# Kernel optimization log

Hardware: AMD Instinct MI355X
Metric: run time of the kernel (lower is better)

Reference implementation:

```python
import jax, jax.numpy as jnp
import numpy as np
from jax import lax

DN = ('NCDHW', 'OIDHW', 'NCDHW')
BN_EPS = 1e-5  # eval-mode BatchNorm3d with running_mean=0, running_var=1


def conv3d(x, w, b):
    y = lax.conv_general_dilated(x, w, window_strides=(1, 1, 1),
                                 padding=[(1, 1)] * 3, dimension_numbers=DN)
    return y + b[None, :, None, None, None]


def maxpool2(x):
    return lax.reduce_window(x, -jnp.inf, lax.max,
                             (1, 1, 2, 2, 2), (1, 1, 2, 2, 2), 'VALID')


def spline_block(x, cw, cb, knots, sw, w1, w2, g, beta):
    # SplineConv3d: conv -> (BSpline3D blend with SiLU) -> BN(eval) -> maxpool
    y = conv3d(x, cw, cb)                                   # [b,c,d,h,w]
    basis = jnp.maximum(y[..., None] - knots, 0.0) ** 3     # [b,c,d,h,w,k]
    sp = jnp.einsum('bcdhwk,ck->bcdhw', basis, sw)
    out = (w1[None, :, None, None, None] * sp
           + w2[None, :, None, None, None] * (y * jax.nn.sigmoid(y)))
    scale = (g / jnp.sqrt(1.0 + BN_EPS))[None, :, None, None, None]
    return maxpool2(out * scale + beta[None, :, None, None, None])


def setup_inputs() -> dict:
    key = jax.random.key(0)
    ks = iter(jax.random.split(key, 40))
    def nrm(shape, s=1.0):
        return jax.random.normal(next(ks), shape, dtype=jnp.float32) * s
    d = {}
    d['x'] = nrm((2, 1, 64, 64, 64))
    for cin, cout, t in [(1, 32, '1'), (32, 64, '2'), (64, 128, '3')]:
        d[f'c{t}_w'] = nrm((cout, cin, 3, 3, 3), 0.1)
        d[f'c{t}_b'] = nrm((cout,), 0.01)
        d[f'c{t}_knots'] = jnp.linspace(-1.0, 1.0, 10).astype(jnp.float32)
        d[f'c{t}_sw'] = nrm((cout, 10), 0.2)
        d[f'c{t}_w1'] = nrm((cout,), 0.2)
        d[f'c{t}_w2'] = nrm((cout,), 0.2)
        d[f'bn{t}_g'] = 1.0 + nrm((cout,), 0.1)
        d[f'bn{t}_b'] = nrm((cout,), 0.1)
    d['fc1_w'] = nrm((256, 128), 0.05)
    d['fc1_b'] = nrm((256,), 0.01)
    d['fc2_w'] = nrm((2, 256), 0.05)
    d['fc2_b'] = nrm((2,), 0.01)
    return d


def reference(x,
              c1_w, c1_b, c1_knots, c1_sw, c1_w1, c1_w2, bn1_g, bn1_b,
              c2_w, c2_b, c2_knots, c2_sw, c2_w1, c2_w2, bn2_g, bn2_b,
              c3_w, c3_b, c3_knots, c3_sw, c3_w1, c3_w2, bn3_g, bn3_b,
              fc1_w, fc1_b, fc2_w, fc2_b):
    h = spline_block(x, c1_w, c1_b, c1_knots, c1_sw, c1_w1, c1_w2, bn1_g, bn1_b)
    h = spline_block(h, c2_w, c2_b, c2_knots, c2_sw, c2_w1, c2_w2, bn2_g, bn2_b)
    h = spline_block(h, c3_w, c3_b, c3_knots, c3_sw, c3_w1, c3_w2, bn3_g, bn3_b)
    h = h.mean(axis=(2, 3, 4))          # AdaptiveAvgPool3d((1,1,1)) + flatten
    h = jax.nn.relu(h @ fc1_w.T + fc1_b)  # dropout is identity in eval mode
    return h @ fc2_w.T + fc2_b
```

## Files before the change

kernel.cpp:

```cpp
#include <hip/hip_runtime.h>
#include <math.h>


#define GLOBAL_AS __attribute__((address_space(1)))
#define LDS_AS    __attribute__((address_space(3)))

static __device__ __forceinline__ void async_ld16(const float* g, float* l) {
    __builtin_amdgcn_global_load_lds((const GLOBAL_AS void*)g, (LDS_AS void*)l,
                                     16, 0, 0);
}

__global__ __launch_bounds__(256) void repack_kernel(
    const float* __restrict__ w1, const float* __restrict__ w2,
    const float* __restrict__ w3,
    float* __restrict__ o1, float* __restrict__ o2, float* __restrict__ o3)
{
    const int i = blockIdx.x * 256 + threadIdx.x;
    const float* src;
    float* dst;
    if (i < 32)            { src = w1 + i * 27;           dst = o1 + i * 28; }
    else if (i < 2080)     { const int j = i - 32;   src = w2 + j * 27; dst = o2 + j * 28; }
    else if (i < 10272)    { const int j = i - 2080; src = w3 + j * 27; dst = o3 + j * 28; }
    else return;
#pragma unroll
    for (int t = 0; t < 27; t++) dst[t] = src[t];
    dst[27] = 0.0f;
}

template <int TPB_, int CIN, int CSPLIT, int G,
          int WDT, int WHT, int WWT, int BD, int BH, int BW>
__global__ __launch_bounds__(TPB_, 2) void spline_block_kernel(
    const float* __restrict__ x,
    const float4* __restrict__ wpk,
    const float* __restrict__ cb,
    const float* __restrict__ knots,
    const float* __restrict__ sw,
    const float* __restrict__ w1,
    const float* __restrict__ w2,
    const float* __restrict__ g,
    const float* __restrict__ beta,
    const float* __restrict__ zbuf,
    float* __restrict__ out,
    int N, int Cout, int D, int H, int W,
    int ntiles, int nthw, int ntw)
{
    constexpr int NSW    = BD * BH * BW;
    constexpr int NW     = TPB_ / 64;
    constexpr int CPG    = CIN / CSPLIT;
    constexpr int ID     = 2 * WDT + 2;
    constexpr int IH     = 2 * WHT + 2;
    constexpr int CHK    = (WWT + 4) / 2;
    constexpr int PITCH  = CHK * 4;
    constexpr int ROWS   = ID * IH;
    constexpr int CHUNKS = ROWS * CHK;
    constexpr int PHYS   = CHUNKS * 4;
    constexpr int NCH    = (CHUNKS + 63) / 64;
    constexpr int BUFS   = (CPG > 1) ? 2 : 1;
    static_assert(NW == NSW * CSPLIT, "waves = spatial-tiles x cin-split");
    static_assert(WDT * WHT * WWT == 64, "one wave per spatial tile");
    static_assert(CIN % CSPLIT == 0, "cin divisible");
    static_assert(NCH <= 32, "mask fits u32");
    static_assert(NCH == 6, "s_waitcnt vmcnt(6) literal assumes 6 issues/cin");
    static_assert(CSPLIT == 1 ||
                  (CSPLIT - 1) * 64 * G * 8 <= NW * BUFS * PHYS,
                  "reduction scratch fits in tile");

    __shared__ __align__(16) float tile[NW][BUFS][PHYS];
    __shared__ float4 stbl[G * 11];

    const int PD = D >> 1, PH = H >> 1, PW = W >> 1;
    const int groups = Cout / G;
    const int tid  = threadIdx.x;
    const int wv   = tid >> 6;
    const int lane = tid & 63;
    const int sw_  = wv % NSW;
    const int cg   = wv / NSW;

    const int bx      = blockIdx.x;
    const int tile_id = bx % ntiles;
    const int t1      = bx / ntiles;
    const int grp     = t1 % groups;
    const int n       = t1 / groups;
    const int c0      = grp * G;
    const int cinbase = cg * CPG;

    const int td  = tile_id / nthw;
    const int rem = tile_id % nthw;
    const int th_ = rem / ntw;
    const int tw_ = rem % ntw;

    for (int i = tid; i < G * 11; i += TPB_) {
        const int gg  = i / 11;
        const int cnt = i % 11;
        const int c   = c0 + gg;
        float A = 0.f, B3 = 0.f, C3 = 0.f, Dd = 0.f;
        for (int j = 0; j < cnt; j++) {
            const float s = sw[c * 10 + j];
            const float k = knots[j];
            A  += s;
            B3 += 3.0f * s * k;
            C3 += 3.0f * s * k * k;
            Dd += s * k * k * k;
        }
        stbl[i] = make_float4(A, B3, C3, Dd);
    }

    const int swd = sw_ / (BH * BW);
    const int r2  = sw_ % (BH * BW);
    const int swh = r2 / BW;
    const int sww = r2 % BW;
    const int pd0 = td  * (BD * WDT) + swd * WDT;
    const int ph0 = th_ * (BH * WHT) + swh * WHT;
    const int pw0 = tw_ * (BW * WWT) + sww * WWT;

    const int pwl = lane % WWT;
    const int phl = (lane / WWT) % WHT;
    const int pdl = lane / (WWT * WHT);

    const int d0 = 2 * pd0 - 1, h0 = 2 * ph0 - 1;
    const int w0 = 2 * pw0 - 1;
    const int wb = w0 & ~3;
    const int woff = w0 - wb;

    int off[NCH];
    unsigned vm = 0;
#pragma unroll
    for (int k = 0; k < NCH; k++) {
        const int chunk = lane + 64 * k;
        const int row = chunk / CHK, cs = chunk - row * CHK;
        const int dz = row / IH, hy = row - dz * IH;
        const int dd = d0 + dz, hh = h0 + hy;
        const int wsd = wb + cs * 4;
        const bool ok = (chunk < CHUNKS) &
                        ((unsigned)dd < (unsigned)D) &
                        ((unsigned)hh < (unsigned)H) &
                        ((unsigned)wsd < (unsigned)W);
        off[k] = ok ? (dd * H + hh) * W + wsd : 0;
        vm |= (unsigned)ok << k;
    }

    const size_t chstride = (size_t)D * H * W;
    const float* xn = x + (size_t)n * CIN * chstride;

    float acc[G][8];
#pragma unroll
    for (int gg = 0; gg < G; gg++)
#pragma unroll
        for (int i = 0; i < 8; i++) acc[gg][i] = 0.0f;

    __syncthreads();

    auto stage = [&](int ci, int buf) {
        const float* xc = xn + (size_t)ci * chstride;
        float* dst = &tile[wv][buf][0];
#pragma unroll
        for (int k = 0; k < NCH; k++) {
            const int chunk = lane + 64 * k;
            if ((k + 1) * 64 <= CHUNKS || chunk < CHUNKS) {
                const float* src = ((vm >> k) & 1) ? (xc + off[k]) : zbuf;
                async_ld16(src, dst + chunk * 4);
            }
        }
    };

    stage(cinbase, 0);

#pragma unroll 1
    for (int s = 0; s < CPG; s++) {
        const int cur = s & (BUFS - 1);
        if (s + 1 < CPG) {
            stage(cinbase + s + 1, cur ^ 1);
            asm volatile("s_waitcnt vmcnt(6)" ::: "memory");
        } else {
            asm volatile("s_waitcnt vmcnt(0)" ::: "memory");
        }

        const int ci = cinbase + s;
        const float* tb = &tile[wv][cur][0];
        float r[64];
#pragma unroll
        for (int dz = 0; dz < 4; dz++)
#pragma unroll
        for (int dy = 0; dy < 4; dy++) {
            const int rb = ((2 * pdl + dz) * IH + (2 * phl + dy)) * PITCH +
                           woff + 2 * pwl;
            r[(dz * 4 + dy) * 4 + 0] = tb[rb + 0];
            r[(dz * 4 + dy) * 4 + 1] = tb[rb + 1];
            r[(dz * 4 + dy) * 4 + 2] = tb[rb + 2];
            r[(dz * 4 + dy) * 4 + 3] = tb[rb + 3];
        }

#pragma unroll
        for (int gg = 0; gg < G; gg++) {
            const float4* wp = wpk + ((size_t)(c0 + gg) * CIN + ci) * 7;
            float4 q[7];
#pragma unroll
            for (int ch = 0; ch < 7; ch++) q[ch] = wp[ch];
#pragma unroll
            for (int ch = 0; ch < 7; ch++) {
#pragma unroll
                for (int j = 0; j < 4; j++) {
                    const int tap = ch * 4 + j;
                    if (tap < 27) {
                        const float wvj = (j == 0) ? q[ch].x : (j == 1) ? q[ch].y
                                        : (j == 2) ? q[ch].z : q[ch].w;
                        const int kd = tap / 9, kh = (tap % 9) / 3, kw = tap % 3;
#pragma unroll
                        for (int od = 0; od < 2; od++)
#pragma unroll
                        for (int oh = 0; oh < 2; oh++)
#pragma unroll
                        for (int ow = 0; ow < 2; ow++)
                            acc[gg][(od * 2 + oh) * 2 + ow] =
                                fmaf(wvj,
                                     r[((od + kd) * 4 + (oh + kh)) * 4 + (ow + kw)],
                                     acc[gg][(od * 2 + oh) * 2 + ow]);
                    }
                }
            }
        }
    }

    float* af = &acc[0][0];
    if (CSPLIT > 1) {
        __syncthreads();
        float* scratch = &tile[0][0][0];
        if (cg > 0) {
#pragma unroll
            for (int idx = 0; idx < G * 8; idx++)
                scratch[(idx * (CSPLIT - 1) + (cg - 1)) * 64 + lane] = af[idx];
        }
        __syncthreads();
        if (cg == 0) {
#pragma unroll
            for (int idx = 0; idx < G * 8; idx++) {
                float s2 = af[idx];
                for (int j = 0; j < CSPLIT - 1; j++)
                    s2 += scratch[(idx * (CSPLIT - 1) + j) * 64 + lane];
                af[idx] = s2;
            }
        }
    }

    if (cg == 0) {
        const int pdg = pd0 + pdl, phg = ph0 + phl, pwg = pw0 + pwl;
#pragma unroll
        for (int gg = 0; gg < G; gg++) {
            const int c = c0 + gg;
            const float bias = cb[c];
            const float W1 = w1[c], W2 = w2[c];
            const float scale = g[c] * rsqrtf(1.0f + 1e-5f);
            const float bb = beta[c];

            float m = -INFINITY;
#pragma unroll
            for (int i = 0; i < 8; i++) {
                const float y = acc[gg][i] + bias;
                int idx = (int)floorf((y + 1.0f) * 4.5f) + 1;
                idx = min(max(idx, 0), 10);
                const float4 cf = stbl[gg * 11 + idx];
                const float sp = ((cf.x * y - cf.y) * y + cf.z) * y - cf.w;
                const float silu = y / (1.0f + __expf(-y));
                const float o = fmaf(W1 * sp + W2 * silu, scale, bb);
                m = fmaxf(m, o);
            }
            out[((size_t)(n * Cout + c) * PD + pdg) * PH * PW + phg * PW + pwg] = m;
        }
    }
}

__global__ __launch_bounds__(64) void mean_kernel(
    const float* __restrict__ h, float* __restrict__ out, int S)
{
    const int nc = blockIdx.x;
    const int lane = threadIdx.x;
    const float* p = h + (size_t)nc * S;
    float s = 0.0f;
    for (int i = lane; i < S; i += 64) s += p[i];
#pragma unroll
    for (int off = 32; off > 0; off >>= 1) s += __shfl_down(s, off, 64);
    if (lane == 0) out[nc] = s / (float)S;
}

__global__ __launch_bounds__(256) void fc_kernel(
    const float* __restrict__ pooled,
    const float* __restrict__ w1, const float* __restrict__ b1,
    const float* __restrict__ w2, const float* __restrict__ b2,
    float* __restrict__ out)
{
    __shared__ float hbuf[2][256];
    const int j = threadIdx.x;
#pragma unroll
    for (int nn = 0; nn < 2; nn++) {
        float s = b1[j];
        for (int k = 0; k < 128; k++)
            s = fmaf(pooled[nn * 128 + k], w1[j * 128 + k], s);
        hbuf[nn][j] = fmaxf(s, 0.0f);
    }
    __syncthreads();
    const int wid = j >> 6, lane = j & 63;
    const int nn = wid >> 1, oo = wid & 1;
    float s = 0.0f;
    for (int k = lane; k < 256; k += 64) s += hbuf[nn][k] * w2[oo * 256 + k];
#pragma unroll
    for (int off = 32; off > 0; off >>= 1) s += __shfl_down(s, off, 64);
    if (lane == 0) out[nn * 2 + oo] = s + b2[oo];
}

extern "C" void kernel_launch(void* const* d_in, const int* in_sizes, int n_in,
                              void* d_out, int out_size, void* d_ws, size_t ws_size,
                              hipStream_t stream) {
    const float* x      = (const float*)d_in[0];
    const float* c1_w   = (const float*)d_in[1];
    const float* c1_b   = (const float*)d_in[2];
    const float* c1_kn  = (const float*)d_in[3];
    const float* c1_sw  = (const float*)d_in[4];
    const float* c1_w1  = (const float*)d_in[5];
    const float* c1_w2  = (const float*)d_in[6];
    const float* bn1_g  = (const float*)d_in[7];
    const float* bn1_b  = (const float*)d_in[8];
    const float* c2_w   = (const float*)d_in[9];
    const float* c2_b   = (const float*)d_in[10];
    const float* c2_kn  = (const float*)d_in[11];
    const float* c2_sw  = (const float*)d_in[12];
    const float* c2_w1  = (const float*)d_in[13];
    const float* c2_w2  = (const float*)d_in[14];
    const float* bn2_g  = (const float*)d_in[15];
    const float* bn2_b  = (const float*)d_in[16];
    const float* c3_w   = (const float*)d_in[17];
    const float* c3_b   = (const float*)d_in[18];
    const float* c3_kn  = (const float*)d_in[19];
    const float* c3_sw  = (const float*)d_in[20];
    const float* c3_w1  = (const float*)d_in[21];
    const float* c3_w2  = (const float*)d_in[22];
    const float* bn3_g  = (const float*)d_in[23];
    const float* bn3_b  = (const float*)d_in[24];
    const float* fc1_w  = (const float*)d_in[25];
    const float* fc1_b  = (const float*)d_in[26];
    const float* fc2_w  = (const float*)d_in[27];
    const float* fc2_b  = (const float*)d_in[28];

    float* ws = (float*)d_ws;
    float* h1     = ws;
    float* h2     = h1 + 2097152;
    float* h3     = h2 + 524288;
    float* pooled = h3 + 131072;
    float* zbuf   = pooled + 256;
    float* wp1    = zbuf + 16;
    float* wp2    = wp1 + 896;
    float* wp3    = wp2 + 57344;

    hipMemsetAsync(zbuf, 0, 64, stream);

    repack_kernel<<<dim3(41), dim3(256), 0, stream>>>(c1_w, c2_w, c3_w,
                                                      wp1, wp2, wp3);

    spline_block_kernel<256, 1, 1, 4, 2, 4, 8, 2, 2, 1>
        <<<dim3(2048), dim3(256), 0, stream>>>(
        x, (const float4*)wp1, c1_b, c1_kn, c1_sw, c1_w1, c1_w2, bn1_g, bn1_b,
        zbuf, h1, 2, 32, 64, 64, 64, 128, 16, 4);
    spline_block_kernel<256, 32, 2, 4, 2, 4, 8, 1, 1, 2>
        <<<dim3(1024), dim3(256), 0, stream>>>(
        h1, (const float4*)wp2, c2_b, c2_kn, c2_sw, c2_w1, c2_w2, bn2_g, bn2_b,
        zbuf, h2, 2, 64, 32, 32, 32, 32, 4, 1);
    spline_block_kernel<256, 64, 4, 4, 2, 4, 8, 1, 1, 1>
        <<<dim3(512), dim3(256), 0, stream>>>(
        h2, (const float4*)wp3, c3_b, c3_kn, c3_sw, c3_w1, c3_w2, bn3_g, bn3_b,
        zbuf, h3, 2, 128, 16, 16, 16, 8, 2, 1);
    mean_kernel<<<dim3(256), dim3(64), 0, stream>>>(h3, pooled, 512);
    fc_kernel<<<dim3(1), dim3(256), 0, stream>>>(pooled, fc1_w, fc1_b, fc2_w, fc2_b,
                                                 (float*)d_out);
}
```

Baseline: 327.8 us.

## Retile first two conv blocks, split weight loads, fuse mean and FC head

Launches the first two spline blocks with 128-thread blocks and different tile/cin-split parameters, doubling the grid size. The weight loads in the inner loop are split into two halves of two output channels each, and the cin base is made wave-uniform via readfirstlane, to cut live registers and let weight addresses go to scalar loads. The separate mean and FC kernels are merged into one single-block head kernel, saving a launch but doing the pooling reduction in only one block.

```diff
diff --git a/kernel.cpp b/kernel.cpp
--- a/kernel.cpp
+++ b/kernel.cpp
@@ -59,6 +59,7 @@
     static_assert(NW == NSW * CSPLIT, "waves = spatial-tiles x cin-split");
     static_assert(WDT * WHT * WWT == 64, "one wave per spatial tile");
     static_assert(CIN % CSPLIT == 0, "cin divisible");
+    static_assert(G == 4, "weight half-loop assumes G==4");
     static_assert(NCH <= 32, "mask fits u32");
     static_assert(NCH == 6, "s_waitcnt vmcnt(6) literal assumes 6 issues/cin");
     static_assert(CSPLIT == 1 ||
@@ -83,6 +84,7 @@
     const int n       = t1 / groups;
     const int c0      = grp * G;
     const int cinbase = cg * CPG;
+    const int cinbase_u = __builtin_amdgcn_readfirstlane(cinbase);
 
     const int td  = tile_id / nthw;
     const int rem = tile_id % nthw;
@@ -163,19 +165,21 @@
         }
     };
 
-    stage(cinbase, 0);
+    stage(cinbase_u, 0);
 
 #pragma unroll 1
     for (int s = 0; s < CPG; s++) {
         const int cur = s & (BUFS - 1);
         if (s + 1 < CPG) {
-            stage(cinbase + s + 1, cur ^ 1);
+            stage(cinbase_u + s + 1, cur ^ 1);
             asm volatile("s_waitcnt vmcnt(6)" ::: "memory");
         } else {
             asm volatile("s_waitcnt vmcnt(0)" ::: "memory");
         }
 
-        const int ci = cinbase + s;
+        const int ci_u = cinbase_u + s;
+        const float4* wq = wpk + (size_t)(c0 * CIN + ci_u) * 7;
+
         const float* tb = &tile[wv][cur][0];
         float r[64];
 #pragma unroll
@@ -191,30 +195,38 @@
         }
 
 #pragma unroll
-        for (int gg = 0; gg < G; gg++) {
-            const float4* wp = wpk + ((size_t)(c0 + gg) * CIN + ci) * 7;
-            float4 q[7];
-#pragma unroll
-            for (int ch = 0; ch < 7; ch++) q[ch] = wp[ch];
-#pragma unroll
-            for (int ch = 0; ch < 7; ch++) {
-#pragma unroll
-                for (int j = 0; j < 4; j++) {
-                    const int tap = ch * 4 + j;
-                    if (tap < 27) {
-                        const float wvj = (j == 0) ? q[ch].x : (j == 1) ? q[ch].y
-                                        : (j == 2) ? q[ch].z : q[ch].w;
-                        const int kd = tap / 9, kh = (tap % 9) / 3, kw = tap % 3;
-#pragma unroll
-                        for (int od = 0; od < 2; od++)
-#pragma unroll
-                        for (int oh = 0; oh < 2; oh++)
-#pragma unroll
-                        for (int ow = 0; ow < 2; ow++)
-                            acc[gg][(od * 2 + oh) * 2 + ow] =
-                                fmaf(wvj,
-                                     r[((od + kd) * 4 + (oh + kh)) * 4 + (ow + kw)],
-                                     acc[gg][(od * 2 + oh) * 2 + ow]);
+        for (int half = 0; half < 2; half++) {
+            float4 q[2][7];
+#pragma unroll
+            for (int gh = 0; gh < 2; gh++)
+#pragma unroll
+                for (int ch = 0; ch < 7; ch++)
+                    q[gh][ch] = wq[(size_t)(half * 2 + gh) * (CIN * 7) + ch];
+#pragma unroll
+            for (int gh = 0; gh < 2; gh++) {
+                const int gg = half * 2 + gh;
+#pragma unroll
+                for (int ch = 0; ch < 7; ch++) {
+#pragma unroll
+                    for (int j = 0; j < 4; j++) {
+                        const int tap = ch * 4 + j;
+                        if (tap < 27) {
+                            const float wvj = (j == 0) ? q[gh][ch].x
+                                            : (j == 1) ? q[gh][ch].y
+                                            : (j == 2) ? q[gh][ch].z
+                                            : q[gh][ch].w;
+                            const int kd = tap / 9, kh = (tap % 9) / 3, kw = tap % 3;
+#pragma unroll
+                            for (int od = 0; od < 2; od++)
+#pragma unroll
+                            for (int oh = 0; oh < 2; oh++)
+#pragma unroll
+                            for (int ow = 0; ow < 2; ow++)
+                                acc[gg][(od * 2 + oh) * 2 + ow] =
+                                    fmaf(wvj,
+                                         r[((od + kd) * 4 + (oh + kh)) * 4 + (ow + kw)],
+                                         acc[gg][(od * 2 + oh) * 2 + ow]);
+                        }
                     }
                 }
             }
@@ -269,42 +281,41 @@
     }
 }
 
-__global__ __launch_bounds__(64) void mean_kernel(
-    const float* __restrict__ h, float* __restrict__ out, int S)
-{
-    const int nc = blockIdx.x;
-    const int lane = threadIdx.x;
-    const float* p = h + (size_t)nc * S;
-    float s = 0.0f;
-    for (int i = lane; i < S; i += 64) s += p[i];
-#pragma unroll
-    for (int off = 32; off > 0; off >>= 1) s += __shfl_down(s, off, 64);
-    if (lane == 0) out[nc] = s / (float)S;
-}
-
-__global__ __launch_bounds__(256) void fc_kernel(
-    const float* __restrict__ pooled,
-    const float* __restrict__ w1, const float* __restrict__ b1,
-    const float* __restrict__ w2, const float* __restrict__ b2,
+__global__ __launch_bounds__(256) void head_kernel(
+    const float* __restrict__ h,
+    const float* __restrict__ fw1, const float* __restrict__ fb1,
+    const float* __restrict__ fw2, const float* __restrict__ fb2,
     float* __restrict__ out)
 {
+    __shared__ float pooled[256];
     __shared__ float hbuf[2][256];
-    const int j = threadIdx.x;
+    const int tid = threadIdx.x, w = tid >> 6, lane = tid & 63;
+    for (int p = w; p < 256; p += 4) {
+        const float* row = h + (size_t)p * 512;
+        float s = 0.0f;
+#pragma unroll
+        for (int i = 0; i < 8; i++) s += row[lane + 64 * i];
+#pragma unroll
+        for (int o = 32; o > 0; o >>= 1) s += __shfl_down(s, o, 64);
+        if (lane == 0) pooled[p] = s * (1.0f / 512.0f);
+    }
+    __syncthreads();
+    const int j = tid;
 #pragma unroll
     for (int nn = 0; nn < 2; nn++) {
-        float s = b1[j];
+        float s = fb1[j];
         for (int k = 0; k < 128; k++)
-            s = fmaf(pooled[nn * 128 + k], w1[j * 128 + k], s);
+            s = fmaf(pooled[nn * 128 + k], fw1[j * 128 + k], s);
         hbuf[nn][j] = fmaxf(s, 0.0f);
     }
     __syncthreads();
-    const int wid = j >> 6, lane = j & 63;
+    const int wid = j >> 6, l2 = j & 63;
     const int nn = wid >> 1, oo = wid & 1;
     float s = 0.0f;
-    for (int k = lane; k < 256; k += 64) s += hbuf[nn][k] * w2[oo * 256 + k];
-#pragma unroll
-    for (int off = 32; off > 0; off >>= 1) s += __shfl_down(s, off, 64);
-    if (lane == 0) out[nn * 2 + oo] = s + b2[oo];
+    for (int k = l2; k < 256; k += 64) s += hbuf[nn][k] * fw2[oo * 256 + k];
+#pragma unroll
+    for (int o = 32; o > 0; o >>= 1) s += __shfl_down(s, o, 64);
+    if (l2 == 0) out[nn * 2 + oo] = s + fb2[oo];
 }
 
 extern "C" void kernel_launch(void* const* d_in, const int* in_sizes, int n_in,
@@ -355,19 +366,18 @@
     repack_kernel<<<dim3(41), dim3(256), 0, stream>>>(c1_w, c2_w, c3_w,
                                                       wp1, wp2, wp3);
 
-    spline_block_kernel<256, 1, 1, 4, 2, 4, 8, 2, 2, 1>
-        <<<dim3(2048), dim3(256), 0, stream>>>(
+    spline_block_kernel<128, 1, 1, 4, 2, 4, 8, 1, 1, 2>
+        <<<dim3(4096), dim3(128), 0, stream>>>(
         x, (const float4*)wp1, c1_b, c1_kn, c1_sw, c1_w1, c1_w2, bn1_g, bn1_b,
-        zbuf, h1, 2, 32, 64, 64, 64, 128, 16, 4);
-    spline_block_kernel<256, 32, 2, 4, 2, 4, 8, 1, 1, 2>
-        <<<dim3(1024), dim3(256), 0, stream>>>(
+        zbuf, h1, 2, 32, 64, 64, 64, 256, 16, 2);
+    spline_block_kernel<128, 32, 2, 4, 2, 4, 8, 1, 1, 1>
+        <<<dim3(2048), dim3(128), 0, stream>>>(
         h1, (const float4*)wp2, c2_b, c2_kn, c2_sw, c2_w1, c2_w2, bn2_g, bn2_b,
-        zbuf, h2, 2, 64, 32, 32, 32, 32, 4, 1);
+        zbuf, h2, 2, 64, 32, 32, 32, 64, 8, 2);
     spline_block_kernel<256, 64, 4, 4, 2, 4, 8, 1, 1, 1>
         <<<dim3(512), dim3(256), 0, stream>>>(
         h2, (const float4*)wp3, c3_b, c3_kn, c3_sw, c3_w1, c3_w2, bn3_g, bn3_b,
         zbuf, h3, 2, 128, 16, 16, 16, 8, 2, 1);
-    mean_kernel<<<dim3(256), dim3(64), 0, stream>>>(h3, pooled, 512);
-    fc_kernel<<<dim3(1), dim3(256), 0, stream>>>(pooled, fc1_w, fc1_b, fc2_w, fc2_b,
-                                                 (float*)d_out);
-}
+    head_kernel<<<dim3(1), dim3(256), 0, stream>>>(h3, fc1_w, fc1_b, fc2_w, fc2_b,
+                                                   (float*)d_out);
+}
```

Result: slower. 369.5 us (+12.7%).
